# Kernel tuning notes

Measured on AMD Instinct MI355X. Metric: run time of the kernel, lower is better.

Reference implementation:

```python
import jax, jax.numpy as jnp
import numpy as np

B, N, DIM, H, D, S = 4, 16384, 256, 8, 64, 64
INNER = H * D


def setup_inputs() -> dict:
    key = jax.random.key(0)
    ks = jax.random.split(key, 10)
    f = lambda k, shp, s: jax.random.normal(k, shp, jnp.float32) * s
    return {
        "x": jax.random.normal(ks[0], (B, N, DIM), jnp.float32),
        "Wx": f(ks[1], (INNER, DIM), 0.02), "bx": jnp.zeros((INNER,), jnp.float32),
        "Wfx": f(ks[2], (INNER, DIM), 0.02), "bfx": jnp.zeros((INNER,), jnp.float32),
        "Wslice": f(ks[3], (S, D), 0.125), "bslice": jnp.zeros((S,), jnp.float32),
        "temperature": jnp.full((1, H, 1, 1), 0.5, jnp.float32),
        "Wq": f(ks[4], (D, D), 0.125),
        "Wk": f(ks[5], (D, D), 0.125),
        "Wv": f(ks[6], (D, D), 0.125),
        "attn_scale": jnp.full((1, H, 1, 1), 10.0, jnp.float32),
        "slice_res_scale": jnp.full((1,), 0.1, jnp.float32),
        "Wout": f(ks[7], (DIM, INNER), 0.02), "bout": jnp.zeros((DIM,), jnp.float32),
    }


def reference(x, Wx, bx, Wfx, bfx, Wslice, bslice, temperature,
              Wq, Wk, Wv, attn_scale, slice_res_scale, Wout, bout):
    b, n, _ = x.shape
    # project and split heads -> [b, h, n, d]
    fx = (x @ Wfx.T + bfx).reshape(b, n, H, D).transpose(0, 2, 1, 3)
    xm = (x @ Wx.T + bx).reshape(b, n, H, D).transpose(0, 2, 1, 3)
    temp = jnp.clip(temperature, 1e-4)
    slice_logits = (xm @ Wslice.T + bslice) / temp              # [b,h,n,S]
    w = jax.nn.softmax(slice_logits, axis=-1)                   # slice weights
    slice_norm = w.sum(axis=2)                                  # [b,h,S]
    tok = jnp.einsum('bhnc,bhng->bhgc', fx, w)                  # [b,h,S,d]
    tok = tok / (slice_norm + 1e-5)[:, :, :, None]
    # small cross-slice attention (cosine, shared kv across heads)
    q = tok @ Wq.T                                              # [b,h,S,d]
    kv = tok.mean(axis=1, keepdims=True)                        # [b,1,S,d]
    k = kv @ Wk.T
    v = kv @ Wv.T
    qn = q / jnp.maximum(jnp.linalg.norm(q, axis=-1, keepdims=True), 1e-12)
    kn = k / jnp.maximum(jnp.linalg.norm(k, axis=-1, keepdims=True), 1e-12)
    logits = jnp.einsum('bhgd,bzsd->bhgs', qn, kn) * attn_scale  # z==1 broadcast
    attn = jax.nn.softmax(logits, axis=-1)
    out_tok = jnp.einsum('bhgs,bzsd->bhgd', attn, v)
    out_tok = out_tok + slice_res_scale * tok
    # broadcast slice tokens back to points
    out_x = jnp.einsum('bhgc,bhng->bhnc', out_tok, w)           # [b,h,n,d]
    out_x = out_x.transpose(0, 2, 1, 3).reshape(b, n, H * D)
    return out_x @ Wout.T + bout
```

## Files before the change

kernel.cpp:

```cpp
#include <hip/hip_runtime.h>
#include <math.h>

#define BQ   4
#define NTOK 16384
#define DIMM 256
#define HH   8
#define DDIM 64
#define SSL  64
#define INNERD 512
#define BN_TOK (BQ*NTOK)

typedef __attribute__((ext_vector_type(8))) short short8;
typedef __attribute__((ext_vector_type(4))) float f32x4;

__device__ inline float bf2f(unsigned short u) {
    union { float f; unsigned int i; } v; v.i = ((unsigned int)u) << 16; return v.f;
}
__device__ inline unsigned short f2bf(float f) {
    union { float f; unsigned int i; } v; v.f = f;
    unsigned int r = v.i + 0x7FFFu + ((v.i >> 16) & 1u);
    return (unsigned short)(r >> 16);
}

__device__ __forceinline__ void gl_lds16(const void* g, void* l) {
    __builtin_amdgcn_global_load_lds(
        (const __attribute__((address_space(1))) unsigned int*)g,
        (__attribute__((address_space(3))) unsigned int*)l, 16, 0, 0);
}

#define WAIT_VM(N) asm volatile("s_waitcnt vmcnt(" #N ")" ::: "memory")
#define WAIT_LGKM0() asm volatile("s_waitcnt lgkmcnt(0)" ::: "memory")

__global__ void k_prep(const float* __restrict__ Wx, const float* __restrict__ bx,
                       const float* __restrict__ Wfx, const float* __restrict__ bfx,
                       const float* __restrict__ Wslice, const float* __restrict__ bslice,
                       unsigned short* __restrict__ Wcatb, float* __restrict__ bcat)
{
    int row = blockIdx.x;
    int t = threadIdx.x;
    if (row < 512) {
        for (int c = t; c < 256; c += 64) Wcatb[row*256 + c] = f2bf(Wfx[row*256 + c]);
        if (t == 0) bcat[row] = bfx[row];
    } else {
        int r = row - 512, h = r >> 6, s = r & 63;
        for (int c = t; c < 256; c += 64) {
            float acc = 0.f;
            for (int d = 0; d < 64; ++d)
                acc += Wslice[s*64 + d] * Wx[(h*64 + d)*256 + c];
            Wcatb[row*256 + c] = f2bf(acc);
        }
        if (t == 0) {
            float acc = bslice[s];
            for (int d = 0; d < 64; ++d) acc += Wslice[s*64 + d] * bx[h*64 + d];
            bcat[row] = acc;
        }
    }
}

__global__ void k_xcast(const float* __restrict__ x, unsigned short* __restrict__ xb)
{
    size_t i = ((size_t)blockIdx.x*256 + threadIdx.x)*8;
    float4 a = *(const float4*)(x + i);
    float4 b = *(const float4*)(x + i + 4);
    *(ushort4*)(xb + i)     = make_ushort4(f2bf(a.x), f2bf(a.y), f2bf(a.z), f2bf(a.w));
    *(ushort4*)(xb + i + 4) = make_ushort4(f2bf(b.x), f2bf(b.y), f2bf(b.z), f2bf(b.w));
}

__global__ __launch_bounds__(256) void k_gemm1(
    const unsigned short* __restrict__ Xb, const unsigned short* __restrict__ Wb,
    const float* __restrict__ bias, const float* __restrict__ temperature,
    unsigned short* __restrict__ fx_t, unsigned short* __restrict__ wbuf)
{
    __shared__ unsigned short As[2][128*32];
    __shared__ unsigned short Bs[2][128*32];
    int bid = blockIdx.x;
    int xcd = bid & 7;
    int inner = bid >> 3;
    int rt = xcd*64 + (inner >> 3);
    int ct = inner & 7;
    int m0 = rt*128, n0 = ct*128;
    int tid = threadIdx.x;
    int lane = tid & 63, w = tid >> 6;
    int wr = w >> 1, wc = w & 1;
    int lr = lane & 15, lq = lane >> 4;

    f32x4 acc[4][4];
#pragma unroll
    for (int i = 0; i < 4; i++)
#pragma unroll
        for (int j = 0; j < 4; j++) acc[i][j] = (f32x4)(0.f);

    int r0 = tid >> 2, kq0 = (tid & 3) * 8;

    auto stage = [&](int buf, int k0) {
        gl_lds16(Xb + (size_t)(m0 + r0)*256 + k0 + kq0,      &As[buf][(size_t)tid*8]);
        gl_lds16(Xb + (size_t)(m0 + 64 + r0)*256 + k0 + kq0, &As[buf][(size_t)(tid+256)*8]);
        gl_lds16(Wb + (size_t)(n0 + r0)*256 + k0 + kq0,      &Bs[buf][(size_t)tid*8]);
        gl_lds16(Wb + (size_t)(n0 + 64 + r0)*256 + k0 + kq0, &Bs[buf][(size_t)(tid+256)*8]);
    };

    stage(0, 0);
    stage(1, 32);
    int cur = 0;
#pragma unroll
    for (int t = 0; t < 8; ++t) {
        if (t < 7) { WAIT_VM(4); } else { WAIT_VM(0); }
        __builtin_amdgcn_s_barrier();
        short8 af[4], bf[4];
#pragma unroll
        for (int i = 0; i < 4; i++) {
            af[i] = *(const short8*)&As[cur][(wr*64 + i*16 + lr)*32 + lq*8];
            bf[i] = *(const short8*)&Bs[cur][(wc*64 + i*16 + lr)*32 + lq*8];
        }
        WAIT_LGKM0();
        __builtin_amdgcn_sched_barrier(0);
        __builtin_amdgcn_s_barrier();
        if (t < 6) stage(cur, (t + 2) * 32);
#pragma unroll
        for (int i = 0; i < 4; i++)
#pragma unroll
            for (int j = 0; j < 4; j++)
                acc[i][j] = __builtin_amdgcn_mfma_f32_16x16x32_bf16(af[i], bf[j], acc[i][j], 0, 0, 0);
        cur ^= 1;
    }

    float bv[4];
#pragma unroll
    for (int j = 0; j < 4; j++) bv[j] = bias[n0 + wc*64 + j*16 + lr];

    if (n0 < 512) {
        int h = (n0 + wc*64) >> 6;
        int batch = m0 >> 14;
#pragma unroll
        for (int i = 0; i < 4; i++) {
            int tokbase = m0 + wr*64 + i*16 + lq*4;
            int nloc = tokbase & (NTOK-1);
#pragma unroll
            for (int j = 0; j < 4; j++) {
                int d = j*16 + lr;
                ushort4 pk = make_ushort4(
                    f2bf(acc[i][j][0] + bv[j]), f2bf(acc[i][j][1] + bv[j]),
                    f2bf(acc[i][j][2] + bv[j]), f2bf(acc[i][j][3] + bv[j]));
                *(ushort4*)(fx_t + ((size_t)(batch*8 + h)*64 + d)*NTOK + nloc) = pk;
            }
        }
    } else {
        int h = (n0 - 512 + wc*64) >> 6;
        float it = 1.f / fmaxf(temperature[h], 1e-4f);
        int colbase = (n0 - 512) + wc*64;
#pragma unroll
        for (int i = 0; i < 4; i++) {
            int tokbase = m0 + wr*64 + i*16 + lq*4;
#pragma unroll
            for (int r = 0; r < 4; r++) {
                float v[4];
#pragma unroll
                for (int j = 0; j < 4; j++) v[j] = (acc[i][j][r] + bv[j]) * it;
                float mx = fmaxf(fmaxf(v[0], v[1]), fmaxf(v[2], v[3]));
                mx = fmaxf(mx, __shfl_xor(mx, 1));
                mx = fmaxf(mx, __shfl_xor(mx, 2));
                mx = fmaxf(mx, __shfl_xor(mx, 4));
                mx = fmaxf(mx, __shfl_xor(mx, 8));
                float e[4], sm = 0.f;
#pragma unroll
                for (int j = 0; j < 4; j++) { e[j] = __expf(v[j] - mx); sm += e[j]; }
                sm += __shfl_xor(sm, 1);
                sm += __shfl_xor(sm, 2);
                sm += __shfl_xor(sm, 4);
                sm += __shfl_xor(sm, 8);
                float inv = 1.f / sm;
                size_t rowoff = (size_t)(tokbase + r)*512 + colbase + lr;
#pragma unroll
                for (int j = 0; j < 4; j++)
                    wbuf[rowoff + j*16] = f2bf(e[j] * inv);
            }
        }
    }
}

__global__ __launch_bounds__(256) void k_tok(
    const unsigned short* __restrict__ wbuf, const unsigned short* __restrict__ fx_t,
    float* __restrict__ tok_acc, float* __restrict__ norm_acc)
{
    __shared__ unsigned short As[2][32*64];
    __shared__ unsigned short Bs[2][64*32];
    int chunk = blockIdx.x;
    int bh = blockIdx.y;
    int b = bh >> 3, h = bh & 7;
    int n0 = chunk * 512;
    int tid = threadIdx.x;
    int lane = tid & 63, w = tid >> 6;
    int lr = lane & 15, lq = lane >> 4;

    f32x4 acc[4];
#pragma unroll
    for (int j = 0; j < 4; j++) acc[j] = (f32x4)(0.f);
    float nacc = 0.f;

    const unsigned short* wsrc =
        wbuf + ((size_t)(b*NTOK + n0 + (tid >> 3)))*512 + h*64 + (tid & 7)*8;
    const unsigned short* fsrc =
        fx_t + ((size_t)bh*64 + (tid >> 2))*NTOK + n0 + (tid & 3)*8;

    auto stage = [&](int buf, int kk) {
        gl_lds16(wsrc + (size_t)kk*512, &As[buf][(size_t)tid*8]);
        gl_lds16(fsrc + kk,             &Bs[buf][(size_t)tid*8]);
    };

    stage(0, 0);
    stage(1, 32);
    int cur = 0;
#pragma unroll
    for (int t = 0; t < 16; ++t) {
        if (t < 15) { WAIT_VM(2); } else { WAIT_VM(0); }
        __builtin_amdgcn_s_barrier();
        const unsigned short* arow = &As[cur][w*16 + lr];
        short8 af;
#pragma unroll
        for (int e = 0; e < 8; ++e)
            af[e] = (short)arow[(lq*8 + e)*64];
        short8 bfv[4];
#pragma unroll
        for (int j = 0; j < 4; j++)
            bfv[j] = *(const short8*)&Bs[cur][(j*16 + lr)*32 + lq*8];
        WAIT_LGKM0();
        __builtin_amdgcn_sched_barrier(0);
        __builtin_amdgcn_s_barrier();
        if (t < 14) stage(cur, (t + 2) * 32);

        float ns = 0.f;
#pragma unroll
        for (int e = 0; e < 8; ++e) ns += bf2f((unsigned short)af[e]);
        nacc += ns;
#pragma unroll
        for (int j = 0; j < 4; j++)
            acc[j] = __builtin_amdgcn_mfma_f32_16x16x32_bf16(af, bfv[j], acc[j], 0, 0, 0);
        cur ^= 1;
    }

#pragma unroll
    for (int j = 0; j < 4; j++) {
        int d = j*16 + lr;
#pragma unroll
        for (int r = 0; r < 4; r++) {
            int s = w*16 + lq*4 + r;
            atomicAdd(&tok_acc[((size_t)bh*64 + s)*64 + d], acc[j][r]);
        }
    }
    nacc += __shfl_xor(nacc, 16);
    nacc += __shfl_xor(nacc, 32);
    if (lq == 0)
        atomicAdd(&norm_acc[bh*64 + w*16 + lr], nacc);
}

__global__ __launch_bounds__(256) void k_kv(
    const float* __restrict__ tok, const float* __restrict__ norm,
    const float* __restrict__ Wk, const float* __restrict__ Wv,
    float* __restrict__ kn_out, float* __restrict__ v_out)
{
    __shared__ float KV[64][65];
    __shared__ float TMP[64][65];
    __shared__ float rn[64];
    __shared__ float inv[8][64];
    int b = blockIdx.x, tid = threadIdx.x;
    for (int idx = tid; idx < 512; idx += 256) {
        int h = idx >> 6, s = idx & 63;
        inv[h][s] = 1.f / (norm[(b*8 + h)*64 + s] + 1e-5f);
    }
    __syncthreads();
    for (int idx = tid; idx < 4096; idx += 256) {
        int s = idx >> 6;
        float acc = 0.f;
        for (int h = 0; h < 8; ++h)
            acc += tok[((size_t)(b*8 + h))*4096 + idx] * inv[h][s];
        KV[s][idx & 63] = acc * 0.125f;
    }
    __syncthreads();
    for (int idx = tid; idx < 4096; idx += 256) {
        int s = idx >> 6, d = idx & 63;
        float a = 0.f;
        for (int e = 0; e < 64; ++e) a += KV[s][e] * Wk[d*64 + e];
        TMP[s][d] = a;
    }
    __syncthreads();
    if (tid < 64) {
        float a = 0.f;
        for (int d = 0; d < 64; ++d) { float x = TMP[tid][d]; a += x*x; }
        rn[tid] = fmaxf(sqrtf(a), 1e-12f);
    }
    __syncthreads();
    for (int idx = tid; idx < 4096; idx += 256) {
        int s = idx >> 6, d = idx & 63;
        kn_out[(size_t)b*4096 + idx] = TMP[s][d] / rn[s];
    }
    for (int idx = tid; idx < 4096; idx += 256) {
        int s = idx >> 6, d = idx & 63;
        float a = 0.f;
        for (int e = 0; e < 64; ++e) a += KV[s][e] * Wv[d*64 + e];
        v_out[(size_t)b*4096 + idx] = a;
    }
}

__global__ __launch_bounds__(256) void k_attn(
    const float* __restrict__ tok, const float* __restrict__ norm,
    const float* __restrict__ Wq,
    const float* __restrict__ kn, const float* __restrict__ vbuf,
    const float* __restrict__ attn_scale, const float* __restrict__ srs,
    float* __restrict__ out_tok)
{
    __shared__ float TN[64][65];
    __shared__ float Q[64][65];
    __shared__ float KN[64][65];
    __shared__ float L[64][65];
    __shared__ float rn[64];
    int h = blockIdx.x & 7, b = blockIdx.x >> 3;
    int bh = b*8 + h;
    int tid = threadIdx.x;
    for (int idx = tid; idx < 4096; idx += 256) {
        int g = idx >> 6;
        TN[g][idx & 63] = tok[(size_t)bh*4096 + idx] / (norm[bh*64 + g] + 1e-5f);
        KN[g][idx & 63] = kn[(size_t)b*4096 + idx];
    }
    __syncthreads();
    for (int idx = tid; idx < 4096; idx += 256) {
        int g = idx >> 6, d = idx & 63;
        float a = 0.f;
        for (int e = 0; e < 64; ++e) a += TN[g][e] * Wq[d*64 + e];
        Q[g][d] = a;
    }
    __syncthreads();
    if (tid < 64) {
        float a = 0.f;
        for (int d = 0; d < 64; ++d) { float x = Q[tid][d]; a += x*x; }
        rn[tid] = fmaxf(sqrtf(a), 1e-12f);
    }
    __syncthreads();
    float scale = attn_scale[h];
    for (int idx = tid; idx < 4096; idx += 256) {
        int g = idx >> 6, s = idx & 63;
        float a = 0.f;
        for (int e = 0; e < 64; ++e) a += Q[g][e] * KN[s][e];
        L[g][s] = a / rn[g] * scale;
    }
    __syncthreads();
    if (tid < 64) {
        float mx = -1e30f;
        for (int s = 0; s < 64; ++s) mx = fmaxf(mx, L[tid][s]);
        float sm = 0.f;
        for (int s = 0; s < 64; ++s) { float e = expf(L[tid][s]-mx); L[tid][s] = e; sm += e; }
        float ivv = 1.f/sm;
        for (int s = 0; s < 64; ++s) L[tid][s] *= ivv;
    }
    __syncthreads();
    float srsv = srs[0];
    for (int idx = tid; idx < 4096; idx += 256) {
        int g = idx >> 6, d = idx & 63;
        float a = 0.f;
        for (int s = 0; s < 64; ++s) a += L[g][s] * vbuf[(size_t)b*4096 + s*64 + d];
        out_tok[(size_t)bh*4096 + idx] = a + srsv * TN[g][d];
    }
}

__global__ __launch_bounds__(256) void k_mt(
    const float* __restrict__ out_tok, const float* __restrict__ Wout,
    unsigned short* __restrict__ MTb)
{
    __shared__ float Wt[64][68];
    __shared__ float Ot[64][68];
    int jt = blockIdx.x, h = blockIdx.y, b = blockIdx.z;
    int j0 = jt * 64;
    int tid = threadIdx.x;
    int tx = tid & 15, ty = tid >> 4;
#pragma unroll
    for (int i = 0; i < 4; i++) {
        int flat = tid + i*256;
        int r = flat >> 4;
        int c4 = (flat & 15) * 4;
        float4 wv = *(const float4*)(Wout + (size_t)(j0+r)*512 + h*64 + c4);
        Wt[c4+0][r]=wv.x; Wt[c4+1][r]=wv.y; Wt[c4+2][r]=wv.z; Wt[c4+3][r]=wv.w;
        float4 ov = *(const float4*)(out_tok + ((size_t)(b*8+h)*64 + r)*64 + c4);
        Ot[c4+0][r]=ov.x; Ot[c4+1][r]=ov.y; Ot[c4+2][r]=ov.z; Ot[c4+3][r]=ov.w;
    }
    __syncthreads();
    float acc[4][4] = {{0.f}};
#pragma unroll 8
    for (int d = 0; d < 64; ++d) {
        float av[4], bv[4];
        *(float4*)av = *(const float4*)&Wt[d][ty*4];
        *(float4*)bv = *(const float4*)&Ot[d][tx*4];
#pragma unroll
        for (int i = 0; i < 4; i++)
#pragma unroll
            for (int j = 0; j < 4; j++) acc[i][j] += av[i]*bv[j];
    }
#pragma unroll
    for (int i = 0; i < 4; i++) {
        int j = j0 + ty*4 + i;
#pragma unroll
        for (int jj = 0; jj < 4; jj++) {
            int s = tx*4 + jj;
            MTb[((size_t)(b*256) + j)*512 + h*64 + s] = f2bf(acc[i][jj]);
        }
    }
}

__global__ __launch_bounds__(256) void k_gemm2(
    const unsigned short* __restrict__ A, const unsigned short* __restrict__ Ball,
    const float* __restrict__ bias, float* __restrict__ C)
{
    __shared__ unsigned short As[2][128*32];
    __shared__ unsigned short Bs[2][128*32];
    int bid = blockIdx.x;
    int xcd = bid & 7;
    int inner = bid >> 3;
    int rt = xcd*64 + (inner >> 1);
    int ct = inner & 1;
    int m0 = rt*128, n0 = ct*128;
    const unsigned short* Bm = Ball + (size_t)(m0 >> 14) * 256 * 512;
    int tid = threadIdx.x;
    int lane = tid & 63, w = tid >> 6;
    int wr = w >> 1, wc = w & 1;
    int lr = lane & 15, lq = lane >> 4;

    f32x4 acc[4][4];
#pragma unroll
    for (int i = 0; i < 4; i++)
#pragma unroll
        for (int j = 0; j < 4; j++) acc[i][j] = (f32x4)(0.f);

    int r0 = tid >> 2, kq0 = (tid & 3) * 8;

    auto stage = [&](int buf, int k0) {
        gl_lds16(A + (size_t)(m0 + r0)*512 + k0 + kq0,       &As[buf][(size_t)tid*8]);
        gl_lds16(A + (size_t)(m0 + 64 + r0)*512 + k0 + kq0,  &As[buf][(size_t)(tid+256)*8]);
        gl_lds16(Bm + (size_t)(n0 + r0)*512 + k0 + kq0,      &Bs[buf][(size_t)tid*8]);
        gl_lds16(Bm + (size_t)(n0 + 64 + r0)*512 + k0 + kq0, &Bs[buf][(size_t)(tid+256)*8]);
    };

    stage(0, 0);
    stage(1, 32);
    int cur = 0;
#pragma unroll
    for (int t = 0; t < 16; ++t) {
        if (t < 15) { WAIT_VM(4); } else { WAIT_VM(0); }
        __builtin_amdgcn_s_barrier();
        short8 af[4], bf[4];
#pragma unroll
        for (int i = 0; i < 4; i++) {
            af[i] = *(const short8*)&As[cur][(wr*64 + i*16 + lr)*32 + lq*8];
            bf[i] = *(const short8*)&Bs[cur][(wc*64 + i*16 + lr)*32 + lq*8];
        }
        WAIT_LGKM0();
        __builtin_amdgcn_sched_barrier(0);
        __builtin_amdgcn_s_barrier();
        if (t < 14) stage(cur, (t + 2) * 32);
#pragma unroll
        for (int i = 0; i < 4; i++)
#pragma unroll
            for (int j = 0; j < 4; j++)
                acc[i][j] = __builtin_amdgcn_mfma_f32_16x16x32_bf16(af[i], bf[j], acc[i][j], 0, 0, 0);
        cur ^= 1;
    }

#pragma unroll
    for (int j = 0; j < 4; j++) {
        int n = n0 + wc*64 + j*16 + lr;
        float bv = bias[n];
#pragma unroll
        for (int i = 0; i < 4; i++) {
            int mrow = m0 + wr*64 + i*16 + lq*4;
#pragma unroll
            for (int r = 0; r < 4; r++)
                C[(size_t)(mrow + r)*256 + n] = acc[i][j][r] + bv;
        }
    }
}

extern "C" void kernel_launch(void* const* d_in, const int* in_sizes, int n_in,
                              void* d_out, int out_size, void* d_ws, size_t ws_size,
                              hipStream_t stream)
{
    const float* x      = (const float*)d_in[0];
    const float* Wx     = (const float*)d_in[1];
    const float* bx     = (const float*)d_in[2];
    const float* Wfx    = (const float*)d_in[3];
    const float* bfx    = (const float*)d_in[4];
    const float* Wslice = (const float*)d_in[5];
    const float* bslice = (const float*)d_in[6];
    const float* temperature = (const float*)d_in[7];
    const float* Wq     = (const float*)d_in[8];
    const float* Wk     = (const float*)d_in[9];
    const float* Wv     = (const float*)d_in[10];
    const float* attn_scale = (const float*)d_in[11];
    const float* srs    = (const float*)d_in[12];
    const float* Wout   = (const float*)d_in[13];
    const float* bout   = (const float*)d_in[14];
    float* out = (float*)d_out;
    float* ws  = (float*)d_ws;

    float* tok  = ws + 0;
    float* norm = ws + 131072;
    float* bcat = ws + 133120;
    float* kn   = ws + 134144;
    float* vb   = ws + 150528;
    float* ot   = ws + 166912;
    unsigned short* Wcatb = (unsigned short*)(ws + 297984);
    unsigned short* MTb   = (unsigned short*)(ws + 429056);
    unsigned short* xb    = (unsigned short*)(ws + 691200);
    unsigned short* wbuf  = (unsigned short*)(ws + 9079808);
    unsigned short* fx_t  = (unsigned short*)d_out;

    hipMemsetAsync(tok, 0, 133120 * sizeof(float), stream);
    k_prep<<<1024, 64, 0, stream>>>(Wx, bx, Wfx, bfx, Wslice, bslice, Wcatb, bcat);
    k_xcast<<<8192, 256, 0, stream>>>(x, xb);
    k_gemm1<<<4096, 256, 0, stream>>>(xb, Wcatb, bcat, temperature, fx_t, wbuf);
    k_tok<<<dim3(32, 32), 256, 0, stream>>>(wbuf, fx_t, tok, norm);
    k_kv<<<4, 256, 0, stream>>>(tok, norm, Wk, Wv, kn, vb);
    k_attn<<<32, 256, 0, stream>>>(tok, norm, Wq, kn, vb, attn_scale, srs, ot);
    k_mt<<<dim3(4, 8, 4), 256, 0, stream>>>(ot, Wout, MTb);
    k_gemm2<<<1024, 256, 0, stream>>>(wbuf, MTb, bout, out);
}
```

Before: 368.7 us.

## Swizzle LDS tiles in GEMM kernels and fuse Wout product into attention kernel

Applies an XOR swizzle to the k-quarter index when staging global-to-LDS tiles in k_gemm1, k_tok and k_gemm2, and applies the same swizzle on the LDS reads. The goal is fewer LDS bank conflicts on the MFMA fragment loads. Separately, the k_mt kernel is folded into k_attn, which now multiplies the output tokens by Wout in a loop over four column tiles. This removes one launch and the global round trip for out_tok, but the fused part runs on only 32 blocks and not 128.

```diff
diff --git a/kernel.cpp b/kernel.cpp
--- a/kernel.cpp
+++ b/kernel.cpp
@@ -83,6 +83,7 @@
     int lane = tid & 63, w = tid >> 6;
     int wr = w >> 1, wc = w & 1;
     int lr = lane & 15, lq = lane >> 4;
+    int lqs = lq ^ ((lr >> 1) & 3);
 
     f32x4 acc[4][4];
 #pragma unroll
@@ -90,13 +91,14 @@
 #pragma unroll
         for (int j = 0; j < 4; j++) acc[i][j] = (f32x4)(0.f);
 
-    int r0 = tid >> 2, kq0 = (tid & 3) * 8;
+    int r0 = tid >> 2;
+    int kswz = (((tid & 3) ^ ((tid >> 3) & 3))) * 8;
 
     auto stage = [&](int buf, int k0) {
-        gl_lds16(Xb + (size_t)(m0 + r0)*256 + k0 + kq0,      &As[buf][(size_t)tid*8]);
-        gl_lds16(Xb + (size_t)(m0 + 64 + r0)*256 + k0 + kq0, &As[buf][(size_t)(tid+256)*8]);
-        gl_lds16(Wb + (size_t)(n0 + r0)*256 + k0 + kq0,      &Bs[buf][(size_t)tid*8]);
-        gl_lds16(Wb + (size_t)(n0 + 64 + r0)*256 + k0 + kq0, &Bs[buf][(size_t)(tid+256)*8]);
+        gl_lds16(Xb + (size_t)(m0 + r0)*256 + k0 + kswz,      &As[buf][(size_t)tid*8]);
+        gl_lds16(Xb + (size_t)(m0 + 64 + r0)*256 + k0 + kswz, &As[buf][(size_t)(tid+256)*8]);
+        gl_lds16(Wb + (size_t)(n0 + r0)*256 + k0 + kswz,      &Bs[buf][(size_t)tid*8]);
+        gl_lds16(Wb + (size_t)(n0 + 64 + r0)*256 + k0 + kswz, &Bs[buf][(size_t)(tid+256)*8]);
     };
 
     stage(0, 0);
@@ -109,8 +111,8 @@
         short8 af[4], bf[4];
 #pragma unroll
         for (int i = 0; i < 4; i++) {
-            af[i] = *(const short8*)&As[cur][(wr*64 + i*16 + lr)*32 + lq*8];
-            bf[i] = *(const short8*)&Bs[cur][(wc*64 + i*16 + lr)*32 + lq*8];
+            af[i] = *(const short8*)&As[cur][(wr*64 + i*16 + lr)*32 + lqs*8];
+            bf[i] = *(const short8*)&Bs[cur][(wc*64 + i*16 + lr)*32 + lqs*8];
         }
         WAIT_LGKM0();
         __builtin_amdgcn_sched_barrier(0);
@@ -191,6 +193,7 @@
     int tid = threadIdx.x;
     int lane = tid & 63, w = tid >> 6;
     int lr = lane & 15, lq = lane >> 4;
+    int lqs = lq ^ ((lr >> 1) & 3);
 
     f32x4 acc[4];
 #pragma unroll
@@ -199,8 +202,9 @@
 
     const unsigned short* wsrc =
         wbuf + ((size_t)(b*NTOK + n0 + (tid >> 3)))*512 + h*64 + (tid & 7)*8;
+    int kswz = (((tid & 3) ^ ((tid >> 3) & 3))) * 8;
     const unsigned short* fsrc =
-        fx_t + ((size_t)bh*64 + (tid >> 2))*NTOK + n0 + (tid & 3)*8;
+        fx_t + ((size_t)bh*64 + (tid >> 2))*NTOK + n0 + kswz;
 
     auto stage = [&](int buf, int kk) {
         gl_lds16(wsrc + (size_t)kk*512, &As[buf][(size_t)tid*8]);
@@ -222,7 +226,7 @@
         short8 bfv[4];
 #pragma unroll
         for (int j = 0; j < 4; j++)
-            bfv[j] = *(const short8*)&Bs[cur][(j*16 + lr)*32 + lq*8];
+            bfv[j] = *(const short8*)&Bs[cur][(j*16 + lr)*32 + lqs*8];
         WAIT_LGKM0();
         __builtin_amdgcn_sched_barrier(0);
         __builtin_amdgcn_s_barrier();
@@ -306,7 +310,7 @@
     const float* __restrict__ Wq,
     const float* __restrict__ kn, const float* __restrict__ vbuf,
     const float* __restrict__ attn_scale, const float* __restrict__ srs,
-    float* __restrict__ out_tok)
+    const float* __restrict__ Wout, unsigned short* __restrict__ MTb)
 {
     __shared__ float TN[64][65];
     __shared__ float Q[64][65];
@@ -357,49 +361,41 @@
         int g = idx >> 6, d = idx & 63;
         float a = 0.f;
         for (int s = 0; s < 64; ++s) a += L[g][s] * vbuf[(size_t)b*4096 + s*64 + d];
-        out_tok[(size_t)bh*4096 + idx] = a + srsv * TN[g][d];
-    }
-}
-
-__global__ __launch_bounds__(256) void k_mt(
-    const float* __restrict__ out_tok, const float* __restrict__ Wout,
-    unsigned short* __restrict__ MTb)
-{
-    __shared__ float Wt[64][68];
-    __shared__ float Ot[64][68];
-    int jt = blockIdx.x, h = blockIdx.y, b = blockIdx.z;
-    int j0 = jt * 64;
-    int tid = threadIdx.x;
+        Q[g][d] = a + srsv * TN[g][d];
+    }
+
     int tx = tid & 15, ty = tid >> 4;
-#pragma unroll
-    for (int i = 0; i < 4; i++) {
-        int flat = tid + i*256;
-        int r = flat >> 4;
-        int c4 = (flat & 15) * 4;
-        float4 wv = *(const float4*)(Wout + (size_t)(j0+r)*512 + h*64 + c4);
-        Wt[c4+0][r]=wv.x; Wt[c4+1][r]=wv.y; Wt[c4+2][r]=wv.z; Wt[c4+3][r]=wv.w;
-        float4 ov = *(const float4*)(out_tok + ((size_t)(b*8+h)*64 + r)*64 + c4);
-        Ot[c4+0][r]=ov.x; Ot[c4+1][r]=ov.y; Ot[c4+2][r]=ov.z; Ot[c4+3][r]=ov.w;
-    }
-    __syncthreads();
-    float acc[4][4] = {{0.f}};
+    for (int jt = 0; jt < 4; ++jt) {
+        __syncthreads();
+#pragma unroll
+        for (int i = 0; i < 4; i++) {
+            int flat = tid + i*256;
+            int r = flat >> 4;
+            int c4 = (flat & 15) * 4;
+            float4 wv = *(const float4*)(Wout + (size_t)(jt*64 + r)*512 + h*64 + c4);
+            KN[c4+0][r]=wv.x; KN[c4+1][r]=wv.y; KN[c4+2][r]=wv.z; KN[c4+3][r]=wv.w;
+        }
+        __syncthreads();
+        float acc2[4][4] = {{0.f}};
 #pragma unroll 8
-    for (int d = 0; d < 64; ++d) {
-        float av[4], bv[4];
-        *(float4*)av = *(const float4*)&Wt[d][ty*4];
-        *(float4*)bv = *(const float4*)&Ot[d][tx*4];
-#pragma unroll
-        for (int i = 0; i < 4; i++)
-#pragma unroll
-            for (int j = 0; j < 4; j++) acc[i][j] += av[i]*bv[j];
-    }
-#pragma unroll
-    for (int i = 0; i < 4; i++) {
-        int j = j0 + ty*4 + i;
-#pragma unroll
-        for (int jj = 0; jj < 4; jj++) {
-            int s = tx*4 + jj;
-            MTb[((size_t)(b*256) + j)*512 + h*64 + s] = f2bf(acc[i][jj]);
+        for (int d = 0; d < 64; ++d) {
+            float av[4], bv[4];
+            *(float4*)av = *(const float4*)&KN[d][ty*4];
+            bv[0] = Q[tx*4+0][d]; bv[1] = Q[tx*4+1][d];
+            bv[2] = Q[tx*4+2][d]; bv[3] = Q[tx*4+3][d];
+#pragma unroll
+            for (int i = 0; i < 4; i++)
+#pragma unroll
+                for (int j = 0; j < 4; j++) acc2[i][j] += av[i]*bv[j];
+        }
+#pragma unroll
+        for (int i = 0; i < 4; i++) {
+            int j = jt*64 + ty*4 + i;
+#pragma unroll
+            for (int jj = 0; jj < 4; jj++) {
+                int s = tx*4 + jj;
+                MTb[((size_t)(b*256) + j)*512 + h*64 + s] = f2bf(acc2[i][jj]);
+            }
         }
     }
 }
@@ -421,6 +417,7 @@
     int lane = tid & 63, w = tid >> 6;
     int wr = w >> 1, wc = w & 1;
     int lr = lane & 15, lq = lane >> 4;
+    int lqs = lq ^ ((lr >> 1) & 3);
 
     f32x4 acc[4][4];
 #pragma unroll
@@ -428,13 +425,14 @@
 #pragma unroll
         for (int j = 0; j < 4; j++) acc[i][j] = (f32x4)(0.f);
 
-    int r0 = tid >> 2, kq0 = (tid & 3) * 8;
+    int r0 = tid >> 2;
+    int kswz = (((tid & 3) ^ ((tid >> 3) & 3))) * 8;
 
     auto stage = [&](int buf, int k0) {
-        gl_lds16(A + (size_t)(m0 + r0)*512 + k0 + kq0,       &As[buf][(size_t)tid*8]);
-        gl_lds16(A + (size_t)(m0 + 64 + r0)*512 + k0 + kq0,  &As[buf][(size_t)(tid+256)*8]);
-        gl_lds16(Bm + (size_t)(n0 + r0)*512 + k0 + kq0,      &Bs[buf][(size_t)tid*8]);
-        gl_lds16(Bm + (size_t)(n0 + 64 + r0)*512 + k0 + kq0, &Bs[buf][(size_t)(tid+256)*8]);
+        gl_lds16(A + (size_t)(m0 + r0)*512 + k0 + kswz,       &As[buf][(size_t)tid*8]);
+        gl_lds16(A + (size_t)(m0 + 64 + r0)*512 + k0 + kswz,  &As[buf][(size_t)(tid+256)*8]);
+        gl_lds16(Bm + (size_t)(n0 + r0)*512 + k0 + kswz,      &Bs[buf][(size_t)tid*8]);
+        gl_lds16(Bm + (size_t)(n0 + 64 + r0)*512 + k0 + kswz, &Bs[buf][(size_t)(tid+256)*8]);
     };
 
     stage(0, 0);
@@ -447,8 +445,8 @@
         short8 af[4], bf[4];
 #pragma unroll
         for (int i = 0; i < 4; i++) {
-            af[i] = *(const short8*)&As[cur][(wr*64 + i*16 + lr)*32 + lq*8];
-            bf[i] = *(const short8*)&Bs[cur][(wc*64 + i*16 + lr)*32 + lq*8];
+            af[i] = *(const short8*)&As[cur][(wr*64 + i*16 + lr)*32 + lqs*8];
+            bf[i] = *(const short8*)&Bs[cur][(wc*64 + i*16 + lr)*32 + lqs*8];
         }
         WAIT_LGKM0();
         __builtin_amdgcn_sched_barrier(0);
@@ -503,7 +501,6 @@
     float* bcat = ws + 133120;
     float* kn   = ws + 134144;
     float* vb   = ws + 150528;
-    float* ot   = ws + 166912;
     unsigned short* Wcatb = (unsigned short*)(ws + 297984);
     unsigned short* MTb   = (unsigned short*)(ws + 429056);
     unsigned short* xb    = (unsigned short*)(ws + 691200);
@@ -516,7 +513,6 @@
     k_gemm1<<<4096, 256, 0, stream>>>(xb, Wcatb, bcat, temperature, fx_t, wbuf);
     k_tok<<<dim3(32, 32), 256, 0, stream>>>(wbuf, fx_t, tok, norm);
     k_kv<<<4, 256, 0, stream>>>(tok, norm, Wk, Wv, kn, vb);
-    k_attn<<<32, 256, 0, stream>>>(tok, norm, Wq, kn, vb, attn_scale, srs, ot);
-    k_mt<<<dim3(4, 8, 4), 256, 0, stream>>>(ot, Wout, MTb);
+    k_attn<<<32, 256, 0, stream>>>(tok, norm, Wq, kn, vb, attn_scale, srs, Wout, MTb);
     k_gemm2<<<1024, 256, 0, stream>>>(wbuf, MTb, bout, out);
 }
```

Measured after the change: 378.2 us. +2.6%, slower.
